# Kernel optimization log

Hardware: AMD Instinct MI355X
Metric: run time of the kernel (lower is better)

The kernel has to match this reference:

```python
import jax, jax.numpy as jnp
import numpy as np

B, K, D, TPE, PPE, HEADS = 8, 128, 128, 64, 64, 8


def setup_inputs() -> dict:
    key = jax.random.key(0)
    ks = jax.random.split(key, 16)
    rn = lambda i, s: jax.random.normal(ks[i], s, dtype=jnp.float32)
    w = lambda i, s: rn(i, s) * 0.05
    z = lambda n: jnp.zeros((n,), jnp.float32)
    return {
        "v_f": rn(0, (B, K, D)),
        "e_f": rn(1, (B, K * K, D)),
        "p_pe": rn(2, (B, K, PPE)),
        "t_pe": rn(3, (B, TPE)),
        "W_vpe": w(4, (D + PPE + TPE, D)), "b_vpe": z(D),
        "W_epe": w(5, (D + TPE, D)), "b_epe": z(D),
        "W_ev1": w(6, (D + 2 * D, D)), "b_ev1": z(D),
        "W_ev2": w(7, (D, D)), "b_ev2": z(D),
        "W_q": w(8, (D, D)), "b_q": z(D),
        "W_k": w(9, (D, D)), "b_k": z(D),
        "W_self": w(10, (D, D)), "b_self": z(D),
        "W_out": w(11, (2 * D, D)), "b_out": z(D),
    }


def reference(v_f, e_f, p_pe, t_pe, W_vpe, b_vpe, W_epe, b_epe, W_ev1, b_ev1,
              W_ev2, b_ev2, W_q, b_q, W_k, b_k, W_self, b_self, W_out, b_out):
    silu = jax.nn.silu
    Bv, Kv, _ = v_f.shape
    t_dim = t_pe.shape[-1]
    # PE binding MLPs
    t_v = jnp.broadcast_to(t_pe[:, None, :], (Bv, Kv, t_dim))
    v = silu(jnp.concatenate([v_f, p_pe, t_v], -1) @ W_vpe + b_vpe)  # [B,K,D]
    t_e = jnp.broadcast_to(t_pe[:, None, :], (Bv, Kv * Kv, t_dim))
    e = silu(jnp.concatenate([e_f, t_e], -1) @ W_epe + b_epe)        # [B,K*K,D]
    Dv = v.shape[-1]
    # pairwise node features + edge feature -> edge value MLP
    e_mtx = e.reshape(Bv, Kv, Kv, -1)
    ev = jnp.concatenate([
        jnp.broadcast_to(v[:, :, None, :], (Bv, Kv, Kv, Dv)),
        jnp.broadcast_to(v[:, None, :, :], (Bv, Kv, Kv, Dv)),
        e_mtx], -1)                                                   # [B,K,K,3D]
    e_value = silu(ev @ W_ev1 + b_ev1) @ W_ev2 + b_ev2                # [B,K,K,E]
    E = e_value.shape[-1]
    G = E // HEADS
    # grouped-head elementwise-QK attention, softmax over neighbor axis (2)
    q = v @ W_q + b_q
    k = v @ W_k + b_k
    scores = (q[:, :, None, :] * k[:, None, :, :]).reshape(Bv, Kv, Kv, G, HEADS)
    scores = scores.sum(-1) / np.float32(np.sqrt(HEADS * 3.0))        # [B,K,K,G]
    atten = jax.nn.softmax(scores, axis=2)
    agg = (atten[..., None] * e_value.reshape(Bv, Kv, Kv, G, HEADS)).sum(2)
    agg = agg.reshape(Bv, Kv, E)
    vf = agg + silu(v @ W_self + b_self)
    pool = jnp.broadcast_to(vf.max(axis=1, keepdims=True), vf.shape)
    v_out = silu(jnp.concatenate([vf, pool], -1) @ W_out + b_out)     # [B,K,Vout]
    return v_out, e_value.reshape(Bv, Kv * Kv, E)
```

## Files before the change

### kernel.cpp

```cpp
#include <hip/hip_runtime.h>
#include <hip/hip_bf16.h>


typedef __attribute__((ext_vector_type(8)))  short bh8;
typedef __attribute__((ext_vector_type(16))) float f16v;
typedef __attribute__((ext_vector_type(4)))  float f4v;

__device__ __forceinline__ unsigned short f2bf(float f) {
  unsigned u = __builtin_bit_cast(unsigned, f);
  u += 0x7fffu + ((u >> 16) & 1u);
  return (unsigned short)(u >> 16);
}
__device__ __forceinline__ float silu_f(float x) {
  float e = __builtin_amdgcn_exp2f(x * -1.44269504088896f);
  return x * __builtin_amdgcn_rcpf(1.f + e);
}
__device__ __forceinline__ bh8 cvt8(f4v x, f4v y) {
  bh8 a;
  a[0] = (short)f2bf(x[0]); a[1] = (short)f2bf(x[1]);
  a[2] = (short)f2bf(x[2]); a[3] = (short)f2bf(x[3]);
  a[4] = (short)f2bf(y[0]); a[5] = (short)f2bf(y[1]);
  a[6] = (short)f2bf(y[2]); a[7] = (short)f2bf(y[3]);
  return a;
}
typedef const __attribute__((address_space(1))) unsigned int gq_t;
typedef __attribute__((address_space(3))) unsigned int lq_t;
__device__ __forceinline__ void gload_lds16(const void* g, void* l) {
  __builtin_amdgcn_global_load_lds((gq_t*)g, (lq_t*)l, 16, 0, 0);
}
__device__ __forceinline__ unsigned fkey(float x) {
  unsigned u = __builtin_bit_cast(unsigned, x);
  return u ^ (((unsigned)((int)u >> 31)) | 0x80000000u);
}
__device__ __forceinline__ float funkey(unsigned key) {
  unsigned u = (key & 0x80000000u) ? (key ^ 0x80000000u) : ~key;
  return __builtin_bit_cast(float, u);
}

__device__ __forceinline__ void wfrag_work(const float* __restrict__ W,
                                           short* __restrict__ dst, int kdim,
                                           int blk, int nblk) {
  int ksteps = kdim >> 4;
  int total  = kdim * 128;
  for (int idx = blk * 256 + threadIdx.x; idx < total; idx += nblk * 256) {
    int jj = idx & 7;
    int l  = (idx >> 3) & 63;
    int rest = idx >> 9;
    int ks = rest % ksteps;
    int ni = rest / ksteps;
    int n  = ni * 32 + (l & 31);
    int kk = ks * 16 + ((l >> 5) << 3) + jj;
    dst[idx] = (short)f2bf(W[kk * 128 + n]);
  }
}

__global__ __launch_bounds__(256) void k_front(
    const float* __restrict__ W_epe, short* __restrict__ wf1,
    const float* __restrict__ W_ev1, short* __restrict__ wf2,
    const float* __restrict__ W_ev2, short* __restrict__ wf3,
    const float* __restrict__ tpe, const float* __restrict__ bepe,
    float* __restrict__ tc, unsigned* __restrict__ poolU,
    const float* __restrict__ vfeat, const float* __restrict__ ppe,
    const float* __restrict__ Wv, const float* __restrict__ bv,
    const float* __restrict__ Wq, const float* __restrict__ bq,
    const float* __restrict__ Wk, const float* __restrict__ bk,
    const float* __restrict__ Ws, const float* __restrict__ bs,
    const float* __restrict__ We, const float* __restrict__ be,
    unsigned short* __restrict__ vb16, float* __restrict__ q,
    float* __restrict__ kb, float* __restrict__ sa, float* __restrict__ evi) {
  const int blk = blockIdx.x;
  if (blk < 260) {
    if (blk < 64)       wfrag_work(W_epe, wf1, 128, blk, 64);
    else if (blk < 192) wfrag_work(W_ev1 + 128 * 128, wf2, 256, blk - 64, 128);
    else if (blk < 256) wfrag_work(W_ev2, wf3, 128, blk - 192, 64);
    else {
      int t = threadIdx.x;
      int b = (blk - 256) * 2 + (t >> 7);
      int n = t & 127;
      float a = bepe[n];
      for (int k2 = 0; k2 < 64; ++k2)
        a += tpe[b * 64 + k2] * W_epe[(128 + k2) * 128 + n];
      tc[b * 128 + n] = a;
    }
    return;
  }
  if (blk == 260) {
    for (int j = threadIdx.x; j < 1024; j += 256) poolU[j] = 0u;
    return;
  }
  __shared__ float x[2][256];
  __shared__ float par[2][2][128];
  __shared__ float xv[2][128];
  const int r0 = (blk - 261) * 2;
  const int b  = r0 >> 7;
  const int t  = threadIdx.x;
  const int c  = t & 127;
  const int hf = t >> 7;
  #pragma unroll
  for (int rr = 0; rr < 2; ++rr) {
    int row = r0 + rr;
    x[rr][t] = (t < 128) ? vfeat[row * 128 + t]
             : (t < 192) ? ppe[row * 64 + (t - 128)]
                         : tpe[b * 64 + (t - 192)];
  }
  __syncthreads();
  {
    float a0 = 0.f, a1 = 0.f;
    const int k0 = hf * 128;
    for (int k4 = k0; k4 < k0 + 128; k4 += 4) {
      f4v x0 = *(const f4v*)&x[0][k4];
      f4v x1 = *(const f4v*)&x[1][k4];
      #pragma unroll
      for (int u = 0; u < 4; ++u) {
        float wv = Wv[(k4 + u) * 128 + c];
        a0 += x0[u] * wv; a1 += x1[u] * wv;
      }
    }
    par[hf][0][c] = a0; par[hf][1][c] = a1;
  }
  __syncthreads();
  if (hf == 0) {
    const float bvv = bv[c];
    #pragma unroll
    for (int rr = 0; rr < 2; ++rr) {
      float s = silu_f(par[0][rr][c] + par[1][rr][c] + bvv);
      vb16[(r0 + rr) * 128 + c] = f2bf(s);
      xv[rr][c] = s;
    }
  }
  __syncthreads();
  const float* WA = hf ? Ws : Wq;
  const float* WB = hf ? We : Wk;
  const float  ba = hf ? bs[c] : bq[c];
  const float  bb = hf ? be[c] : bk[c];
  float aA[2] = {ba, ba}, aB[2] = {bb, bb};
  for (int k4 = 0; k4 < 128; k4 += 4) {
    f4v x0 = *(const f4v*)&xv[0][k4];
    f4v x1 = *(const f4v*)&xv[1][k4];
    #pragma unroll
    for (int u = 0; u < 4; ++u) {
      float wa = WA[(k4 + u) * 128 + c];
      float wb = WB[(k4 + u) * 128 + c];
      aA[0] += x0[u] * wa; aA[1] += x1[u] * wa;
      aB[0] += x0[u] * wb; aB[1] += x1[u] * wb;
    }
  }
  if (hf == 0) {
    #pragma unroll
    for (int rr = 0; rr < 2; ++rr) {
      q[(r0 + rr) * 128 + c]  = aA[rr];
      kb[(r0 + rr) * 128 + c] = aB[rr];
    }
  } else {
    #pragma unroll
    for (int rr = 0; rr < 2; ++rr) {
      sa[(r0 + rr) * 128 + c]  = silu_f(aA[rr]);
      evi[(r0 + rr) * 128 + c] = aB[rr];
    }
  }
}

__global__ __launch_bounds__(256) void k_atten(
    const float* __restrict__ q, const float* __restrict__ kmat,
    float* __restrict__ atten) {
  __shared__ float qr[2][128];
  __shared__ float s[2][128][17];
  __shared__ float red[2][8][17];
  __shared__ float gmax[2][16];
  __shared__ float gsum[2][16];
  const int tid = threadIdx.x;
  const int hi  = tid >> 7;
  const int tt  = tid & 127;
  const int bi  = blockIdx.x * 2 + hi;
  const int b   = bi >> 7;
  qr[hi][tt] = q[(size_t)bi * 128 + tt];
  __syncthreads();
  const float sc = 0.20412414523193154f;
  float loc[16];
  const float* krow = kmat + (size_t)(b * 128 + tt) * 128;
  #pragma unroll
  for (int g = 0; g < 16; ++g) {
    f4v k0 = *(const f4v*)&krow[g * 8];
    f4v k1 = *(const f4v*)&krow[g * 8 + 4];
    float a = 0.f;
    #pragma unroll
    for (int h = 0; h < 4; ++h)
      a += qr[hi][g * 8 + h] * k0[h] + qr[hi][g * 8 + 4 + h] * k1[h];
    loc[g] = a * sc;
    s[hi][tt][g] = loc[g];
  }
  __syncthreads();
  { int g = tt & 15, c = tt >> 4;
    float m = -1e30f;
    for (int j2 = c * 16; j2 < c * 16 + 16; ++j2) m = fmaxf(m, s[hi][j2][g]);
    red[hi][c][g] = m; }
  __syncthreads();
  if (tt < 16) {
    float m = red[hi][0][tt];
    #pragma unroll
    for (int c = 1; c < 8; ++c) m = fmaxf(m, red[hi][c][tt]);
    gmax[hi][tt] = m;
  }
  __syncthreads();
  #pragma unroll
  for (int g = 0; g < 16; ++g) {
    loc[g] = __builtin_amdgcn_exp2f((loc[g] - gmax[hi][g]) * 1.44269504088896f);
    s[hi][tt][g] = loc[g];
  }
  __syncthreads();
  { int g = tt & 15, c = tt >> 4;
    float m = 0.f;
    for (int j2 = c * 16; j2 < c * 16 + 16; ++j2) m += s[hi][j2][g];
    red[hi][c][g] = m; }
  __syncthreads();
  if (tt < 16) {
    float m = 0.f;
    #pragma unroll
    for (int c = 0; c < 8; ++c) m += red[hi][c][tt];
    gsum[hi][tt] = m;
  }
  __syncthreads();
  float* ab = atten + (size_t)bi * 2048 + (size_t)tt * 16;
  #pragma unroll
  for (int g = 0; g < 16; ++g) ab[g] = loc[g] * __builtin_amdgcn_rcpf(gsum[hi][g]);
}

__global__ __launch_bounds__(256) void k_edge(
    const float* __restrict__ ef, const unsigned short* __restrict__ vb,
    const short* __restrict__ wf1, const short* __restrict__ wf2,
    const short* __restrict__ wf3, const float* __restrict__ tc,
    const float* __restrict__ evic, const float* __restrict__ bev2,
    const float* __restrict__ atten, const float* __restrict__ sab,
    float* __restrict__ oute, float* __restrict__ vfb,
    unsigned* __restrict__ poolU) {
  __shared__ __align__(16) unsigned short wbuf0[4096];
  __shared__ __align__(16) unsigned short wbuf1[4096];
  __shared__ __align__(16) unsigned short hbuf[128 * 136];
  const int bi  = ((blockIdx.x & 7) << 7) | (blockIdx.x >> 3);
  const int b   = bi >> 7;
  const int tid = threadIdx.x;
  const int w   = tid >> 6;
  const int l   = tid & 63;
  const int row = w * 32 + (l & 31);
  const int kh  = (l >> 5) << 3;
  const int cb  = l & 31;
  const int rb  = w * 32 + ((l >> 5) << 2);

  const float* efr = ef + (size_t)(bi * 128 + row) * 128;
  const unsigned short* vj = vb + (size_t)(b * 128 + row) * 128;

  auto stage2 = [&](const short* wfp, int KST, int kc, unsigned short* dstb) {
    #pragma unroll
    for (int it = 0; it < 2; ++it) {
      int g  = it * 4 + w;
      int ni = g & 3, kso = g >> 2;
      const short* src = wfp + ((size_t)(ni * KST + kc * 2 + kso) * 64 + l) * 8;
      gload_lds16(src, dstb + g * 512);
    }
  };
  f16v acc[4];
  auto compute2 = [&](const unsigned short* ws2, bh8 aa, bh8 ab2) {
    #pragma unroll
    for (int ni = 0; ni < 4; ++ni) {
      bh8 b0 = *(const bh8*)&ws2[ni * 512 + l * 8];
      acc[ni] = __builtin_amdgcn_mfma_f32_32x32x16_bf16(aa, b0, acc[ni], 0, 0, 0);
    }
    #pragma unroll
    for (int ni = 0; ni < 4; ++ni) {
      bh8 b1 = *(const bh8*)&ws2[(4 + ni) * 512 + l * 8];
      acc[ni] = __builtin_amdgcn_mfma_f32_32x32x16_bf16(ab2, b1, acc[ni], 0, 0, 0);
    }
  };
  auto ldA = [&](int t) -> bh8 {
    if (t < 8) {
      const float* p = efr + t * 16 + kh;
      f4v x0 = *(const f4v*)p;
      f4v x1 = *(const f4v*)(p + 4);
      return cvt8(x0, x1);
    } else if (t < 16) {
      return *(const bh8*)(vj + (t - 8) * 16 + kh);
    } else if (t < 24) {
      return *(const bh8*)&hbuf[row * 136 + (t - 16) * 16 + kh];
    } else {
      return *(const bh8*)&hbuf[row * 136 + (t - 24) * 16 + kh];
    }
  };

  float tin[4], ein[4];
  #pragma unroll
  for (int ni = 0; ni < 4; ++ni) {
    tin[ni] = tc[b * 128 + ni * 32 + cb];
    ein[ni] = evic[bi * 128 + ni * 32 + cb];
  }
  #pragma unroll
  for (int ni = 0; ni < 4; ++ni)
    #pragma unroll
    for (int r = 0; r < 16; ++r) acc[ni][r] = tin[ni];

  stage2(wf1, 8, 0, wbuf0);
  bh8 a0c = ldA(0), a1c = ldA(1);
  __syncthreads();

  #pragma unroll
  for (int c = 0; c < 16; ++c) {
    if (c + 1 < 16) {
      const short* wp; int KST, kc;
      if (c + 1 < 4)       { wp = wf1; KST = 8;  kc = c + 1; }
      else if (c + 1 < 12) { wp = wf2; KST = 16; kc = c + 1 - 4; }
      else                 { wp = wf3; KST = 8;  kc = c + 1 - 12; }
      stage2(wp, KST, kc, (c & 1) ? wbuf0 : wbuf1);
    }
    bh8 a0n, a1n;
    const bool pre = (c + 1 < 16) && (c != 11);
    if (pre) { a0n = ldA(2 * (c + 1)); a1n = ldA(2 * (c + 1) + 1); }
    compute2((c & 1) ? wbuf1 : wbuf0, a0c, a1c);
    if (c == 3) {
      #pragma unroll
      for (int ni = 0; ni < 4; ++ni) {
        int n = ni * 32 + cb;
        #pragma unroll
        for (int r = 0; r < 16; ++r) {
          int rj = rb + (r & 3) + ((r >> 2) << 3);
          hbuf[rj * 136 + n] = f2bf(silu_f(acc[ni][r]));
          acc[ni][r] = ein[ni];
        }
      }
    }
    if (c == 11) {
      #pragma unroll
      for (int ni = 0; ni < 4; ++ni) {
        int n = ni * 32 + cb;
        #pragma unroll
        for (int r = 0; r < 16; ++r) {
          int rj = rb + (r & 3) + ((r >> 2) << 3);
          hbuf[rj * 136 + n] = f2bf(silu_f(acc[ni][r]));
          acc[ni][r] = 0.f;
        }
      }
      a0c = ldA(24); a1c = ldA(25);
    } else if (pre) {
      a0c = a0n; a1c = a1n;
    }
    __syncthreads();
  }

  #pragma unroll
  for (int ni = 0; ni < 4; ++ni) {
    int n = ni * 32 + cb;
    float bv = bev2[n];
    #pragma unroll
    for (int r = 0; r < 16; ++r) {
      int rj = rb + (r & 3) + ((r >> 2) << 3);
      acc[ni][r] += bv;
      oute[(size_t)(bi * 128 + rj) * 128 + n] = acc[ni][r];
    }
  }

  __syncthreads();
  float* attf = (float*)hbuf;
  float* aggl = attf + 2048;
  const float* ap = atten + (size_t)bi * 2048;
  #pragma unroll
  for (int u = 0; u < 8; ++u) {
    int idx = u * 256 + tid;
    float v = ap[idx];
    int j2 = idx >> 4, g = idx & 15;
    attf[j2 * 16 + (g & 3) * 4 + (g >> 2)] = v;
  }
  float sav = 0.f;
  if (tid < 128) sav = sab[(size_t)bi * 128 + tid];
  __syncthreads();
  float p0 = 0.f, p1 = 0.f, p2 = 0.f, p3 = 0.f;
  const int gl = (l & 31) >> 3;
  #pragma unroll
  for (int r = 0; r < 16; ++r) {
    int rj = rb + (r & 3) + ((r >> 2) << 3);
    f4v av = *(const f4v*)&attf[rj * 16 + gl * 4];
    p0 += av[0] * acc[0][r]; p1 += av[1] * acc[1][r];
    p2 += av[2] * acc[2][r]; p3 += av[3] * acc[3][r];
  }
  p0 += __shfl_xor(p0, 32); p1 += __shfl_xor(p1, 32);
  p2 += __shfl_xor(p2, 32); p3 += __shfl_xor(p3, 32);
  if (l < 32) {
    aggl[w * 128 +  0 + l] = p0;
    aggl[w * 128 + 32 + l] = p1;
    aggl[w * 128 + 64 + l] = p2;
    aggl[w * 128 + 96 + l] = p3;
  }
  __syncthreads();
  if (tid < 128) {
    float vf = aggl[tid] + aggl[128 + tid] + aggl[256 + tid] + aggl[384 + tid] + sav;
    vfb[(size_t)bi * 128 + tid] = vf;
    atomicMax(&poolU[b * 128 + tid], fkey(vf));
  }
}

__global__ __launch_bounds__(256) void k_out(
    const float* __restrict__ vfb, const unsigned* __restrict__ poolU,
    const float* __restrict__ W, const float* __restrict__ bias,
    float* __restrict__ vout) {
  __shared__ float x[2][256];
  __shared__ float par[2][2][128];
  const int r0 = blockIdx.x * 2;
  const int b  = r0 >> 7;
  const int t  = threadIdx.x;
  const int c  = t & 127;
  const int hf = t >> 7;
  #pragma unroll
  for (int rr = 0; rr < 2; ++rr)
    x[rr][t] = (t < 128) ? vfb[(r0 + rr) * 128 + t]
                         : funkey(poolU[b * 128 + (t - 128)]);
  __syncthreads();
  {
    float a0 = 0.f, a1 = 0.f;
    const int k0 = hf * 128;
    for (int k4 = k0; k4 < k0 + 128; k4 += 4) {
      f4v x0 = *(const f4v*)&x[0][k4];
      f4v x1 = *(const f4v*)&x[1][k4];
      #pragma unroll
      for (int u = 0; u < 4; ++u) {
        float wv = W[(k4 + u) * 128 + c];
        a0 += x0[u] * wv; a1 += x1[u] * wv;
      }
    }
    par[hf][0][c] = a0; par[hf][1][c] = a1;
  }
  __syncthreads();
  if (hf == 0) {
    const float bvv = bias[c];
    #pragma unroll
    for (int rr = 0; rr < 2; ++rr)
      vout[(r0 + rr) * 128 + c] = silu_f(par[0][rr][c] + par[1][rr][c] + bvv);
  }
}

extern "C" void kernel_launch(void* const* d_in, const int* in_sizes, int n_in,
                              void* d_out, int out_size, void* d_ws, size_t ws_size,
                              hipStream_t stream) {
  const float* v_f    = (const float*)d_in[0];
  const float* e_f    = (const float*)d_in[1];
  const float* p_pe   = (const float*)d_in[2];
  const float* t_pe   = (const float*)d_in[3];
  const float* W_vpe  = (const float*)d_in[4];
  const float* b_vpe  = (const float*)d_in[5];
  const float* W_epe  = (const float*)d_in[6];
  const float* b_epe  = (const float*)d_in[7];
  const float* W_ev1  = (const float*)d_in[8];
  const float* b_ev1  = (const float*)d_in[9];
  const float* W_ev2  = (const float*)d_in[10];
  const float* b_ev2  = (const float*)d_in[11];
  const float* W_q    = (const float*)d_in[12];
  const float* b_q    = (const float*)d_in[13];
  const float* W_k    = (const float*)d_in[14];
  const float* b_k    = (const float*)d_in[15];
  const float* W_self = (const float*)d_in[16];
  const float* b_self = (const float*)d_in[17];
  const float* W_out  = (const float*)d_in[18];
  const float* b_out  = (const float*)d_in[19];

  char* ws = (char*)d_ws;
  unsigned short* vb16  = (unsigned short*)(ws + 0);
  float*          qbuf  = (float*)(ws + 262144);
  float*          kbuf  = (float*)(ws + 786432);
  float*          sabuf = (float*)(ws + 1310720);
  float*          vfbuf = (float*)(ws + 1835008);
  float*          evic  = (float*)(ws + 2359296);
  unsigned*       poolU = (unsigned*)(ws + 2883584);
  float*          tc    = (float*)(ws + 2887680);
  short*          wf1   = (short*)(ws + 2891776);
  short*          wf2   = (short*)(ws + 2924544);
  short*          wf3   = (short*)(ws + 2990080);
  float*          atten = (float*)(ws + 3022848);

  float* v_out = (float*)d_out;
  float* out_e = (float*)d_out + 131072;

  k_front<<<773, 256, 0, stream>>>(W_epe, wf1, W_ev1, wf2, W_ev2, wf3,
                                   t_pe, b_epe, tc, poolU,
                                   v_f, p_pe, W_vpe, b_vpe, W_q, b_q,
                                   W_k, b_k, W_self, b_self, W_ev1, b_ev1,
                                   vb16, qbuf, kbuf, sabuf, evic);
  k_atten<<<512, 256, 0, stream>>>(qbuf, kbuf, atten);
  k_edge<<<1024, 256, 0, stream>>>(e_f, vb16, wf1, wf2, wf3, tc, evic,
                                   b_ev2, atten, sabuf, out_e, vfbuf, poolU);
  k_out<<<512, 256, 0, stream>>>(vfbuf, poolU, W_out, b_out, v_out);
}
```

Before: 77.90 us.

## Preload whole first-layer weight into LDS and deepen weight staging pipeline

The first edge-MLP weight block (wf1) is now loaded into LDS all at once, using the hbuf area before that buffer is needed for activations. This removes the per-chunk syncs for the first phase. The remaining phases prefetch two chunks ahead into the double buffers, with the staging moved after the barrier. The single generic loop is split into three specialised loops, which removes runtime branching in ldA. Risks are an LDS aliasing hazard, since hbuf is reused for both weights and activations, and higher register pressure from the larger unrolled code.

Result: no change. 76.46 us, median of 3 (-1.8%).

```diff
diff --git a/kernel.cpp b/kernel.cpp
--- a/kernel.cpp
+++ b/kernel.cpp
@@ -271,20 +271,20 @@
       acc[ni] = __builtin_amdgcn_mfma_f32_32x32x16_bf16(ab2, b1, acc[ni], 0, 0, 0);
     }
   };
-  auto ldA = [&](int t) -> bh8 {
-    if (t < 8) {
-      const float* p = efr + t * 16 + kh;
-      f4v x0 = *(const f4v*)p;
-      f4v x1 = *(const f4v*)(p + 4);
-      return cvt8(x0, x1);
-    } else if (t < 16) {
-      return *(const bh8*)(vj + (t - 8) * 16 + kh);
-    } else if (t < 24) {
-      return *(const bh8*)&hbuf[row * 136 + (t - 16) * 16 + kh];
-    } else {
-      return *(const bh8*)&hbuf[row * 136 + (t - 24) * 16 + kh];
-    }
+  auto ldAef = [&](int t) -> bh8 {
+    const float* p = efr + t * 16 + kh;
+    f4v x0 = *(const f4v*)p;
+    f4v x1 = *(const f4v*)(p + 4);
+    return cvt8(x0, x1);
   };
+
+  #pragma unroll
+  for (int it = 0; it < 8; ++it) {
+    int s = it * 4 + w;
+    gload_lds16(wf1 + ((size_t)s * 64 + l) * 8, hbuf + s * 512);
+  }
+  stage2(wf2, 16, 0, wbuf0);
+  stage2(wf2, 16, 1, wbuf1);
 
   float tin[4], ein[4];
   #pragma unroll
@@ -297,51 +297,81 @@
     #pragma unroll
     for (int r = 0; r < 16; ++r) acc[ni][r] = tin[ni];
 
-  stage2(wf1, 8, 0, wbuf0);
-  bh8 a0c = ldA(0), a1c = ldA(1);
-  __syncthreads();
-
-  #pragma unroll
-  for (int c = 0; c < 16; ++c) {
-    if (c + 1 < 16) {
-      const short* wp; int KST, kc;
-      if (c + 1 < 4)       { wp = wf1; KST = 8;  kc = c + 1; }
-      else if (c + 1 < 12) { wp = wf2; KST = 16; kc = c + 1 - 4; }
-      else                 { wp = wf3; KST = 8;  kc = c + 1 - 12; }
-      stage2(wp, KST, kc, (c & 1) ? wbuf0 : wbuf1);
-    }
+  bh8 a0c = ldAef(0), a1c = ldAef(1);
+  __syncthreads();
+
+  #pragma unroll
+  for (int p2 = 0; p2 < 4; ++p2) {
     bh8 a0n, a1n;
-    const bool pre = (c + 1 < 16) && (c != 11);
-    if (pre) { a0n = ldA(2 * (c + 1)); a1n = ldA(2 * (c + 1) + 1); }
-    compute2((c & 1) ? wbuf1 : wbuf0, a0c, a1c);
-    if (c == 3) {
-      #pragma unroll
-      for (int ni = 0; ni < 4; ++ni) {
-        int n = ni * 32 + cb;
-        #pragma unroll
-        for (int r = 0; r < 16; ++r) {
-          int rj = rb + (r & 3) + ((r >> 2) << 3);
-          hbuf[rj * 136 + n] = f2bf(silu_f(acc[ni][r]));
-          acc[ni][r] = ein[ni];
-        }
-      }
-    }
-    if (c == 11) {
-      #pragma unroll
-      for (int ni = 0; ni < 4; ++ni) {
-        int n = ni * 32 + cb;
-        #pragma unroll
-        for (int r = 0; r < 16; ++r) {
-          int rj = rb + (r & 3) + ((r >> 2) << 3);
-          hbuf[rj * 136 + n] = f2bf(silu_f(acc[ni][r]));
-          acc[ni][r] = 0.f;
-        }
-      }
-      a0c = ldA(24); a1c = ldA(25);
-    } else if (pre) {
-      a0c = a0n; a1c = a1n;
-    }
+    if (p2 < 3) { a0n = ldAef(2 * p2 + 2); a1n = ldAef(2 * p2 + 3); }
+    #pragma unroll
+    for (int ni = 0; ni < 4; ++ni) {
+      bh8 b0 = *(const bh8*)&hbuf[(ni * 8 + 2 * p2) * 512 + l * 8];
+      acc[ni] = __builtin_amdgcn_mfma_f32_32x32x16_bf16(a0c, b0, acc[ni], 0, 0, 0);
+    }
+    #pragma unroll
+    for (int ni = 0; ni < 4; ++ni) {
+      bh8 b1 = *(const bh8*)&hbuf[(ni * 8 + 2 * p2 + 1) * 512 + l * 8];
+      acc[ni] = __builtin_amdgcn_mfma_f32_32x32x16_bf16(a1c, b1, acc[ni], 0, 0, 0);
+    }
+    if (p2 < 3) { a0c = a0n; a1c = a1n; }
+  }
+  __syncthreads();
+
+  #pragma unroll
+  for (int ni = 0; ni < 4; ++ni) {
+    int n = ni * 32 + cb;
+    #pragma unroll
+    for (int r = 0; r < 16; ++r) {
+      int rj = rb + (r & 3) + ((r >> 2) << 3);
+      hbuf[rj * 136 + n] = f2bf(silu_f(acc[ni][r]));
+      acc[ni][r] = ein[ni];
+    }
+  }
+  a0c = *(const bh8*)(vj + kh);
+  a1c = *(const bh8*)(vj + 16 + kh);
+
+  #pragma unroll
+  for (int c2 = 0; c2 < 8; ++c2) {
+    bh8 a0n, a1n;
+    if (c2 < 7) {
+      const int t0 = 10 + 2 * c2, t1 = t0 + 1;
+      a0n = (t0 < 16) ? *(const bh8*)(vj + (t0 - 8) * 16 + kh)
+                      : *(const bh8*)&hbuf[row * 136 + (t0 - 16) * 16 + kh];
+      a1n = (t1 < 16) ? *(const bh8*)(vj + (t1 - 8) * 16 + kh)
+                      : *(const bh8*)&hbuf[row * 136 + (t1 - 16) * 16 + kh];
+    }
+    compute2((c2 & 1) ? wbuf1 : wbuf0, a0c, a1c);
+    if (c2 < 7) { a0c = a0n; a1c = a1n; }
     __syncthreads();
+    if (c2 + 2 < 8)       stage2(wf2, 16, c2 + 2, (c2 & 1) ? wbuf1 : wbuf0);
+    else if (c2 + 2 < 12) stage2(wf3, 8, c2 + 2 - 8, (c2 & 1) ? wbuf1 : wbuf0);
+  }
+
+  #pragma unroll
+  for (int ni = 0; ni < 4; ++ni) {
+    int n = ni * 32 + cb;
+    #pragma unroll
+    for (int r = 0; r < 16; ++r) {
+      int rj = rb + (r & 3) + ((r >> 2) << 3);
+      hbuf[rj * 136 + n] = f2bf(silu_f(acc[ni][r]));
+      acc[ni][r] = 0.f;
+    }
+  }
+  a0c = *(const bh8*)&hbuf[row * 136 + kh];
+  a1c = *(const bh8*)&hbuf[row * 136 + 16 + kh];
+
+  #pragma unroll
+  for (int c3 = 0; c3 < 4; ++c3) {
+    bh8 a0n, a1n;
+    if (c3 < 3) {
+      a0n = *(const bh8*)&hbuf[row * 136 + (2 * c3 + 2) * 16 + kh];
+      a1n = *(const bh8*)&hbuf[row * 136 + (2 * c3 + 3) * 16 + kh];
+    }
+    compute2((c3 & 1) ? wbuf1 : wbuf0, a0c, a1c);
+    if (c3 < 3) { a0c = a0n; a1c = a1n; }
+    __syncthreads();
+    if (c3 + 2 < 4) stage2(wf3, 8, c3 + 2, (c3 & 1) ? wbuf1 : wbuf0);
   }
 
   #pragma unroll
```
